# Kernel tuning notes

Hardware: AMD Instinct MI355X
Metric: run time of the kernel (lower is better)

The kernel has to match this reference:

```python
import jax, jax.numpy as jnp
import numpy as np

N = 10000
E = 80000


def gat_layer(x, src, dst, W, a_src, a_dst, b):
    # x: [N, Fin], W: [Fin, Fout]
    xw = x @ W                              # [N, Fout]
    al_src = xw @ a_src                     # [N]
    al_dst = xw @ a_dst                     # [N]
    e = jax.nn.leaky_relu(al_src[src] + al_dst[dst], 0.2)  # [E+N]
    m = jax.lax.stop_gradient(jax.ops.segment_max(e, dst, num_segments=N))
    ex = jnp.exp(e - m[dst])
    denom = jax.ops.segment_sum(ex, dst, num_segments=N)
    alpha = ex / (denom[dst] + 1e-16)       # PyG softmax eps
    out = jax.ops.segment_sum(alpha[:, None] * xw[src], dst, num_segments=N)
    return out + b


def setup_inputs() -> dict:
    key = jax.random.key(0)
    ks = jax.random.split(key, 12)
    x = jax.random.normal(ks[0], (N, 256), dtype=jnp.float32)
    edge_index = jax.random.randint(ks[1], (2, E), 0, N, dtype=jnp.int64)
    def glorot(k, fi, fo):
        return jax.random.normal(k, (fi, fo), jnp.float32) * jnp.sqrt(2.0 / (fi + fo))
    W1 = glorot(ks[2], 256, 2048)
    W2 = glorot(ks[3], 2048, 2048)
    W3 = glorot(ks[4], 2048, 1024)
    a1s = jax.random.normal(ks[5], (2048,), jnp.float32) * 0.05
    a1d = jax.random.normal(ks[6], (2048,), jnp.float32) * 0.05
    a2s = jax.random.normal(ks[7], (2048,), jnp.float32) * 0.05
    a2d = jax.random.normal(ks[8], (2048,), jnp.float32) * 0.05
    a3s = jax.random.normal(ks[9], (1024,), jnp.float32) * 0.05
    a3d = jax.random.normal(ks[10], (1024,), jnp.float32) * 0.05
    b1 = jnp.zeros((2048,), jnp.float32)
    b2 = jnp.zeros((2048,), jnp.float32)
    b3 = jnp.zeros((1024,), jnp.float32)
    return {"x": x, "edge_index": edge_index, "W1": W1, "W2": W2, "W3": W3,
            "a1s": a1s, "a1d": a1d, "a2s": a2s, "a2d": a2d, "a3s": a3s, "a3d": a3d,
            "b1": b1, "b2": b2, "b3": b3}


def reference(x, edge_index, W1, W2, W3, a1s, a1d, a2s, a2d, a3s, a3d, b1, b2, b3):
    # add self loops (PyG GATConv default add_self_loops=True)
    loop = jnp.arange(N, dtype=edge_index.dtype)
    src = jnp.concatenate([edge_index[0], loop])
    dst = jnp.concatenate([edge_index[1], loop])
    h = jax.nn.relu(gat_layer(x, src, dst, W1, a1s, a1d, b1))
    h = jax.nn.relu(gat_layer(h, src, dst, W2, a2s, a2d, b2))
    h = jax.nn.relu(gat_layer(h, src, dst, W3, a3s, a3d, b3))
    # F.normalize(dim=1), eps=1e-12
    norm = jnp.linalg.norm(h, axis=1, keepdims=True)
    return h / jnp.maximum(norm, 1e-12)
```

## Files before the change

kernel.cpp:

```cpp
#include <hip/hip_runtime.h>
#include <hip/hip_bf16.h>
#include <math.h>


typedef __attribute__((ext_vector_type(8))) short short8;
typedef __attribute__((ext_vector_type(4))) float f32x4;

#define GLOAD_LDS16(g, l)                                            \
  __builtin_amdgcn_global_load_lds(                                  \
      (const __attribute__((address_space(1))) void*)(g),            \
      (__attribute__((address_space(3))) void*)(l), 16, 0, 0)

__device__ __forceinline__ float bf16_to_f32(ushort u) {
  return __uint_as_float(((unsigned int)u) << 16);
}

__device__ __forceinline__ float block_reduce_sum_bcast(float v) {
#pragma unroll
  for (int off = 32; off > 0; off >>= 1) v += __shfl_down(v, off, 64);
  __shared__ float tmp[4];
  __shared__ float res;
  int lane = threadIdx.x & 63, w = threadIdx.x >> 6;
  if (lane == 0) tmp[w] = v;
  __syncthreads();
  if (threadIdx.x == 0) res = tmp[0] + tmp[1] + tmp[2] + tmp[3];
  __syncthreads();
  float out = res;
  __syncthreads();
  return out;
}

__device__ __forceinline__ float block_reduce_max_bcast(float v) {
#pragma unroll
  for (int off = 32; off > 0; off >>= 1) v = fmaxf(v, __shfl_down(v, off, 64));
  __shared__ float tmpm[4];
  __shared__ float resm;
  int lane = threadIdx.x & 63, w = threadIdx.x >> 6;
  if (lane == 0) tmpm[w] = v;
  __syncthreads();
  if (threadIdx.x == 0) resm = fmaxf(fmaxf(tmpm[0], tmpm[1]), fmaxf(tmpm[2], tmpm[3]));
  __syncthreads();
  float out = resm;
  __syncthreads();
  return out;
}

__global__ void detect_kernel(const int* __restrict__ ei32, int* __restrict__ flag) {
  __shared__ int cnt;
  if (threadIdx.x == 0) cnt = 0;
  __syncthreads();
  int zeros = 0;
  for (int i = threadIdx.x; i < 1024; i += 256) {
    if (ei32[2 * i + 1] == 0) zeros++;
  }
  atomicAdd(&cnt, zeros);
  __syncthreads();
  if (threadIdx.x == 0) *flag = (cnt > 900) ? 1 : 0;
}

__global__ void convert_kernel(const void* __restrict__ ei, const int* __restrict__ flag,
                               int E, int* __restrict__ src, int* __restrict__ dst) {
  int i = blockIdx.x * blockDim.x + threadIdx.x;
  if (i >= E) return;
  if (*flag) {
    const long long* p = (const long long*)ei;
    src[i] = (int)p[i];
    dst[i] = (int)p[E + i];
  } else {
    const int* p = (const int*)ei;
    src[i] = p[i];
    dst[i] = p[E + i];
  }
}

__global__ __launch_bounds__(256) void convert_f32_bf16(const float* __restrict__ in,
                                                        __hip_bfloat16* __restrict__ out,
                                                        int n) {
  int i = blockIdx.x * blockDim.x + threadIdx.x;
  if (i < n) out[i] = __float2bfloat16(in[i]);
}

__global__ __launch_bounds__(256) void transpose_w(const float* __restrict__ W,
                                                   __hip_bfloat16* __restrict__ Wt,
                                                   int K, int Nout) {
  __shared__ float t[32][33];
  int tx = threadIdx.x & 31, ty = threadIdx.x >> 5;
  int n0 = blockIdx.x * 32, k0 = blockIdx.y * 32;
#pragma unroll
  for (int i = 0; i < 4; ++i) {
    int k = k0 + ty + i * 8;
    t[ty + i * 8][tx] = W[(size_t)k * Nout + n0 + tx];
  }
  __syncthreads();
#pragma unroll
  for (int i = 0; i < 4; ++i) {
    int n = n0 + ty + i * 8;
    Wt[(size_t)n * K + k0 + tx] = __float2bfloat16(t[tx][ty + i * 8]);
  }
}

__global__ __launch_bounds__(256) void matvec_wa(const float* __restrict__ W,
                                                 const float* __restrict__ a_s,
                                                 const float* __restrict__ a_d,
                                                 float* __restrict__ wa_s,
                                                 float* __restrict__ wa_d, int F) {
  int k = blockIdx.x;
  const float* row = W + (size_t)k * F;
  float s1 = 0.f, s2 = 0.f;
  for (int f = threadIdx.x; f < F; f += 256) {
    float w = row[f];
    s1 += w * a_s[f];
    s2 += w * a_d[f];
  }
  float r1 = block_reduce_sum_bcast(s1);
  float r2 = block_reduce_sum_bcast(s2);
  if (threadIdx.x == 0) {
    wa_s[k] = r1;
    wa_d[k] = r2;
  }
}

template <int FPT>
__global__ __launch_bounds__(256) void compute_al(const ushort* __restrict__ H,
                                                  const float* __restrict__ wa_s,
                                                  const float* __restrict__ wa_d,
                                                  float* __restrict__ als,
                                                  float* __restrict__ ald, int F) {
  int n = blockIdx.x;
  const ushort* row = H + (size_t)n * F;
  float s1 = 0.f, s2 = 0.f;
  if (FPT == 8) {
    int base = threadIdx.x * 8;
    short8 v = *(const short8*)(row + base);
#pragma unroll
    for (int j = 0; j < 8; ++j) {
      float f = bf16_to_f32((ushort)v[j]);
      s1 += f * wa_s[base + j];
      s2 += f * wa_d[base + j];
    }
  } else {
    float f = bf16_to_f32(row[threadIdx.x]);
    s1 = f * wa_s[threadIdx.x];
    s2 = f * wa_d[threadIdx.x];
  }
  float r1 = block_reduce_sum_bcast(s1);
  float r2 = block_reduce_sum_bcast(s2);
  if (threadIdx.x == 0) {
    als[n] = r1;
    ald[n] = r2;
  }
}

__global__ void count_kernel(const int* __restrict__ dst, int* __restrict__ counts, int E) {
  int i = blockIdx.x * blockDim.x + threadIdx.x;
  if (i < E) atomicAdd(&counts[dst[i]], 1);
}

__global__ __launch_bounds__(1024) void scan_kernel(const int* __restrict__ counts,
                                                    int* __restrict__ rowptr,
                                                    int* __restrict__ cursor, int Nn) {
  __shared__ int part[1024];
  int tid = threadIdx.x;
  int chunk = (Nn + 1023) / 1024;
  int base = tid * chunk;
  int s = 0;
  for (int i = 0; i < chunk; ++i) {
    int idx = base + i;
    if (idx < Nn) s += counts[idx];
  }
  part[tid] = s;
  __syncthreads();
  for (int off = 1; off < 1024; off <<= 1) {
    int v = 0;
    if (tid >= off) v = part[tid - off];
    __syncthreads();
    if (tid >= off) part[tid] += v;
    __syncthreads();
  }
  int run = (tid == 0) ? 0 : part[tid - 1];
  for (int i = 0; i < chunk; ++i) {
    int idx = base + i;
    if (idx < Nn) {
      rowptr[idx] = run;
      cursor[idx] = run;
      run += counts[idx];
    }
  }
  if (tid == 1023) rowptr[Nn] = part[1023];
}

__global__ void fill_kernel(const int* __restrict__ src, const int* __restrict__ dst,
                            int* __restrict__ cursor, int* __restrict__ eidx, int E) {
  int i = blockIdx.x * blockDim.x + threadIdx.x;
  if (i < E) {
    int pos = atomicAdd(&cursor[dst[i]], 1);
    eidx[pos] = src[i];
  }
}

template <int FPT>
__global__ __launch_bounds__(256) void aggregate(const ushort* __restrict__ H,
                                                 const float* __restrict__ als,
                                                 const float* __restrict__ ald,
                                                 const int* __restrict__ rowptr,
                                                 const int* __restrict__ eidx,
                                                 ushort* __restrict__ out, int F) {
  int n = blockIdx.x;
  int tid = threadIdx.x;
  int beg = rowptr[n], end = rowptr[n + 1];
  int deg = end - beg;
  float aldn = ald[n];

  float lm = -INFINITY;
  for (int j = tid; j < deg; j += 256) {
    int s = eidx[beg + j];
    float e = als[s] + aldn;
    e = (e > 0.f) ? e : 0.2f * e;
    lm = fmaxf(lm, e);
  }
  if (tid == 0) {
    float e = als[n] + aldn;
    e = (e > 0.f) ? e : 0.2f * e;
    lm = fmaxf(lm, e);
  }
  float m = block_reduce_max_bcast(lm);

  float ls = 0.f;
  for (int j = tid; j < deg; j += 256) {
    int s = eidx[beg + j];
    float e = als[s] + aldn;
    e = (e > 0.f) ? e : 0.2f * e;
    ls += expf(e - m);
  }
  if (tid == 0) {
    float e = als[n] + aldn;
    e = (e > 0.f) ? e : 0.2f * e;
    ls += expf(e - m);
  }
  float denom = block_reduce_sum_bcast(ls) + 1e-16f;
  float inv_denom = 1.f / denom;

  float acc[FPT];
#pragma unroll
  for (int i = 0; i < FPT; ++i) acc[i] = 0.f;

  __shared__ float alpha_sh[256];
  __shared__ int src_sh[256];
  int total = deg + 1;
  for (int c0 = 0; c0 < total; c0 += 256) {
    int j = c0 + tid;
    if (j < total) {
      int s = (j < deg) ? eidx[beg + j] : n;
      float e = als[s] + aldn;
      e = (e > 0.f) ? e : 0.2f * e;
      alpha_sh[tid] = expf(e - m) * inv_denom;
      src_sh[tid] = s;
    }
    __syncthreads();
    int cn = min(256, total - c0);
    for (int jj = 0; jj < cn; ++jj) {
      float al = alpha_sh[jj];
      const ushort* row = H + (size_t)src_sh[jj] * F;
      if (FPT == 1) {
        acc[0] += al * bf16_to_f32(row[tid]);
      } else {
#pragma unroll
        for (int i = 0; i < FPT / 2; ++i) {
          unsigned int u = *(const unsigned int*)(row + tid * 2 + i * 512);
          acc[2 * i]     += al * __uint_as_float((u & 0xffffu) << 16);
          acc[2 * i + 1] += al * __uint_as_float(u & 0xffff0000u);
        }
      }
    }
    __syncthreads();
  }

#pragma unroll
  for (int i = 0; i < FPT; ++i) {
    int col = (FPT == 1) ? tid : (tid * 2 + (i >> 1) * 512 + (i & 1));
    __hip_bfloat16 hv = __float2bfloat16(acc[i]);
    out[(size_t)n * F + col] = *(ushort*)&hv;
  }
}

template <bool BF16OUT>
__global__ __launch_bounds__(512, 2) void gemm_bn128(const ushort* __restrict__ A,
                                                     const ushort* __restrict__ Bt,
                                                     const float* __restrict__ bias,
                                                     void* __restrict__ C,
                                                     int M, int K, int Nout) {
  constexpr int BUF = 16384 + 8192;
  extern __shared__ ushort lds[];
  const int tid = threadIdx.x;
  const int l = tid & 63, w = tid >> 6;
  const int wm = w >> 2, wn = w & 3;
  const int l15 = l & 15, lhi = l >> 4;

  int nwg = gridDim.x * gridDim.y;
  int lin = blockIdx.y * gridDim.x + blockIdx.x;
  if ((nwg & 7) == 0) lin = (lin & 7) * (nwg >> 3) + (lin >> 3);
  const int bx = lin % gridDim.x, by = lin / gridDim.x;
  const int row0 = by * 256, col0 = bx * 128;

  const int c8sw = (l & 3) ^ (((l >> 5) & 1) << 1);
  const int lrow = l >> 2;
  const int chsw = lhi ^ (((l15 >> 3) & 1) << 1);
  const int rd_off = l15 * 32 + chsw * 8;

  const int sA0 = wm * 8 + wn * 2;
  const int sB0 = w;
  const ushort* ga[2][2];
  const ushort* gb[2];
#pragma unroll
  for (int sc = 0; sc < 2; ++sc) {
#pragma unroll
    for (int j = 0; j < 2; ++j) {
      int ar = min(row0 + (sA0 + j) * 16 + lrow, M - 1);
      ga[sc][j] = A + (size_t)ar * K + sc * 32 + c8sw * 8;
    }
    gb[sc] = Bt + (size_t)(col0 + sB0 * 16 + lrow) * K + sc * 32 + c8sw * 8;
  }

#define STAGE_PH(nb, kn, sc)                                                         \
  do {                                                                               \
    GLOAD_LDS16(ga[sc][0] + (kn), &lds[(nb)*BUF + ((sA0 + 0) * 2 + (sc)) * 512]);    \
    GLOAD_LDS16(ga[sc][1] + (kn), &lds[(nb)*BUF + ((sA0 + 1) * 2 + (sc)) * 512]);    \
    GLOAD_LDS16(gb[sc] + (kn), &lds[(nb)*BUF + 16384 + (sB0 * 2 + (sc)) * 512]);     \
  } while (0)

  f32x4 acc[8][2] = {};

#define PHASE(cbase, kk, STAGE_STMT)                                                 \
  do {                                                                               \
    short8 af[8], bf[2];                                                             \
    _Pragma("unroll") for (int m = 0; m < 8; ++m)                                    \
        af[m] = *(const short8*)(cbase + ((wm * 8 + m) * 2 + (kk)) * 512 + rd_off);  \
    _Pragma("unroll") for (int n = 0; n < 2; ++n)                                    \
        bf[n] = *(const short8*)(cbase + 16384 + ((wn * 2 + n) * 2 + (kk)) * 512 + rd_off); \
    STAGE_STMT;                                                                      \
    asm volatile("s_waitcnt vmcnt(6)" ::: "memory");                                 \
    __builtin_amdgcn_s_barrier();                                                    \
    __builtin_amdgcn_s_setprio(1);                                                   \
    _Pragma("unroll") for (int m = 0; m < 8; ++m)                                    \
        _Pragma("unroll") for (int n = 0; n < 2; ++n)                                \
            acc[m][n] = __builtin_amdgcn_mfma_f32_16x16x32_bf16(                     \
                af[m], bf[n], acc[m][n], 0, 0, 0);                                   \
    __builtin_amdgcn_s_setprio(0);                                                   \
    __builtin_amdgcn_s_barrier();                                                    \
  } while (0)

  const int nt = K >> 6;
  STAGE_PH(0, 0, 0);
  STAGE_PH(0, 0, 1);
  STAGE_PH(1, 64, 0);
  STAGE_PH(1, 64, 1);
  asm volatile("s_waitcnt vmcnt(6)" ::: "memory");
  __builtin_amdgcn_s_barrier();

  int cur = 0;
  for (int t = 0; t < nt; ++t) {
    const ushort* cb = &lds[cur * BUF];
    int nb = cur + 2; if (nb >= 3) nb -= 3;
    const bool pf = (t + 2) < nt;
    const int kn = (t + 2) << 6;
    PHASE(cb, 0, if (pf) STAGE_PH(nb, kn, 0));
    PHASE(cb, 1, if (pf) STAGE_PH(nb, kn, 1));
    cur = cur + 1; if (cur == 3) cur = 0;
  }

#pragma unroll
  for (int mi = 0; mi < 8; ++mi) {
#pragma unroll
    for (int v = 0; v < 4; ++v) {
      int r = row0 + wm * 128 + mi * 16 + lhi * 4 + v;
      if (r < M) {
#pragma unroll
        for (int n = 0; n < 2; ++n) {
          int col = col0 + wn * 32 + n * 16 + l15;
          float val = fmaxf(acc[mi][n][v] + bias[col], 0.f);
          size_t idx = (size_t)r * Nout + col;
          if (BF16OUT)
            ((__hip_bfloat16*)C)[idx] = __float2bfloat16(val);
          else
            ((float*)C)[idx] = val;
        }
      }
    }
  }
#undef PHASE
#undef STAGE_PH
}

__global__ __launch_bounds__(256) void normalize_kernel(const float* __restrict__ h,
                                                        float* __restrict__ out,
                                                        int F) {
  int n = blockIdx.x;
  const float* row = h + (size_t)n * F;
  float ss = 0.f;
  for (int f = threadIdx.x; f < F; f += 256) {
    float v = row[f];
    ss += v * v;
  }
  float tot = block_reduce_sum_bcast(ss);
  float inv = 1.f / fmaxf(sqrtf(tot), 1e-12f);
  for (int f = threadIdx.x; f < F; f += 256) {
    out[(size_t)n * F + f] = row[f] * inv;
  }
}

extern "C" void kernel_launch(void* const* d_in, const int* in_sizes, int n_in,
                              void* d_out, int out_size, void* d_ws, size_t ws_size,
                              hipStream_t stream) {
  const float* x   = (const float*)d_in[0];
  const void*  ei  = d_in[1];
  const float* W1  = (const float*)d_in[2];
  const float* W2  = (const float*)d_in[3];
  const float* W3  = (const float*)d_in[4];
  const float* a1s = (const float*)d_in[5];
  const float* a1d = (const float*)d_in[6];
  const float* a2s = (const float*)d_in[7];
  const float* a2d = (const float*)d_in[8];
  const float* a3s = (const float*)d_in[9];
  const float* a3d = (const float*)d_in[10];
  const float* b1  = (const float*)d_in[11];
  const float* b2  = (const float*)d_in[12];
  const float* b3  = (const float*)d_in[13];

  const int N = in_sizes[0] / 256;
  const int E = in_sizes[1] / 2;

  char* ws = (char*)d_ws;
  size_t off = 0;
  auto alloc = [&](size_t bytes) -> void* {
    void* p = ws + off;
    off += (bytes + 255) & ~(size_t)255;
    return p;
  };
  ushort* h    = (ushort*)alloc((size_t)N * 2048 * 2);
  ushort* hagg = (ushort*)alloc((size_t)N * 2048 * 2);
  float* hf32  = (float*)alloc((size_t)N * 1024 * 4);
  ushort* xb   = (ushort*)alloc((size_t)N * 256 * 2);
  __hip_bfloat16* Wt1 = (__hip_bfloat16*)alloc((size_t)2048 * 256 * 2);
  __hip_bfloat16* Wt2 = (__hip_bfloat16*)alloc((size_t)2048 * 2048 * 2);
  __hip_bfloat16* Wt3 = (__hip_bfloat16*)alloc((size_t)1024 * 2048 * 2);
  float* wa1s = (float*)alloc(256 * 4);
  float* wa1d = (float*)alloc(256 * 4);
  float* wa2s = (float*)alloc(2048 * 4);
  float* wa2d = (float*)alloc(2048 * 4);
  float* wa3s = (float*)alloc(2048 * 4);
  float* wa3d = (float*)alloc(2048 * 4);
  float* als   = (float*)alloc((size_t)N * 4);
  float* ald   = (float*)alloc((size_t)N * 4);
  int* counts  = (int*)alloc((size_t)N * 4);
  int* rowptr  = (int*)alloc((size_t)(N + 1) * 4);
  int* cursor  = (int*)alloc((size_t)N * 4);
  int* eidx    = (int*)alloc((size_t)E * 4);
  int* src32   = (int*)alloc((size_t)E * 4);
  int* dst32   = (int*)alloc((size_t)E * 4);
  int* flag    = (int*)alloc(256);

  static bool attr_done = false;
  if (!attr_done) {
    hipFuncSetAttribute((const void*)gemm_bn128<true>,
                        hipFuncAttributeMaxDynamicSharedMemorySize, 147456);
    hipFuncSetAttribute((const void*)gemm_bn128<false>,
                        hipFuncAttributeMaxDynamicSharedMemorySize, 147456);
    attr_done = true;
  }

  detect_kernel<<<1, 256, 0, stream>>>((const int*)ei, flag);
  convert_kernel<<<(E + 255) / 256, 256, 0, stream>>>(ei, flag, E, src32, dst32);
  hipMemsetAsync(counts, 0, (size_t)N * 4, stream);
  count_kernel<<<(E + 255) / 256, 256, 0, stream>>>(dst32, counts, E);
  scan_kernel<<<1, 1024, 0, stream>>>(counts, rowptr, cursor, N);
  fill_kernel<<<(E + 255) / 256, 256, 0, stream>>>(src32, dst32, cursor, eidx, E);

  convert_f32_bf16<<<(N * 256 + 255) / 256, 256, 0, stream>>>(x, (__hip_bfloat16*)xb, N * 256);
  transpose_w<<<dim3(2048 / 32, 256 / 32), 256, 0, stream>>>(W1, Wt1, 256, 2048);
  transpose_w<<<dim3(2048 / 32, 2048 / 32), 256, 0, stream>>>(W2, Wt2, 2048, 2048);
  transpose_w<<<dim3(1024 / 32, 2048 / 32), 256, 0, stream>>>(W3, Wt3, 2048, 1024);
  matvec_wa<<<256, 256, 0, stream>>>(W1, a1s, a1d, wa1s, wa1d, 2048);
  matvec_wa<<<2048, 256, 0, stream>>>(W2, a2s, a2d, wa2s, wa2d, 2048);
  matvec_wa<<<2048, 256, 0, stream>>>(W3, a3s, a3d, wa3s, wa3d, 1024);

  dim3 blk(256);
  dim3 gblk(512);
  int mb = (N + 255) / 256;

  compute_al<1><<<N, blk, 0, stream>>>(xb, wa1s, wa1d, als, ald, 256);
  aggregate<1><<<N, blk, 0, stream>>>(xb, als, ald, rowptr, eidx, hagg, 256);
  gemm_bn128<true><<<dim3(2048 / 128, mb), gblk, 147456, stream>>>(hagg, (const ushort*)Wt1, b1, h, N, 256, 2048);

  compute_al<8><<<N, blk, 0, stream>>>(h, wa2s, wa2d, als, ald, 2048);
  aggregate<8><<<N, blk, 0, stream>>>(h, als, ald, rowptr, eidx, hagg, 2048);
  gemm_bn128<true><<<dim3(2048 / 128, mb), gblk, 147456, stream>>>(hagg, (const ushort*)Wt2, b2, h, N, 2048, 2048);

  compute_al<8><<<N, blk, 0, stream>>>(h, wa3s, wa3d, als, ald, 2048);
  aggregate<8><<<N, blk, 0, stream>>>(h, als, ald, rowptr, eidx, hagg, 2048);
  gemm_bn128<false><<<dim3(1024 / 128, mb), gblk, 147456, stream>>>(hagg, (const ushort*)Wt3, b3, hf32, N, 2048, 1024);

  normalize_kernel<<<N, blk, 0, stream>>>(hf32, (float*)d_out, 1024);
}
```

Baseline: 473.9 us.

## Restructure GEMM pipeline to five-stage K=32 buffers with deeper prefetch

Replaces the three-buffer, K=64-per-stage GEMM pipeline (two phases per stage) with a five-buffer ring of K=32 stages, prefetching four stages ahead. The barrier and vmcnt wait now come before the LDS fragment reads, and the tail phases use decreasing wait counts. The goal is more loads in flight and less time stalled on global-to-LDS latency. The cost is a per-block LDS size (122880 bytes) that still permits only one block per CU (launch bounds changed to 1), and one barrier pair per 32-wide K step.

```diff
diff --git a/kernel.cpp b/kernel.cpp
--- a/kernel.cpp
+++ b/kernel.cpp
@@ -10,6 +10,8 @@
   __builtin_amdgcn_global_load_lds(                                  \
       (const __attribute__((address_space(1))) void*)(g),            \
       (__attribute__((address_space(3))) void*)(l), 16, 0, 0)
+
+#define CFENCE asm volatile("" ::: "memory")
 
 __device__ __forceinline__ float bf16_to_f32(ushort u) {
   return __uint_as_float(((unsigned int)u) << 16);
@@ -284,12 +286,12 @@
 }
 
 template <bool BF16OUT>
-__global__ __launch_bounds__(512, 2) void gemm_bn128(const ushort* __restrict__ A,
-                                                     const ushort* __restrict__ Bt,
-                                                     const float* __restrict__ bias,
-                                                     void* __restrict__ C,
-                                                     int M, int K, int Nout) {
-  constexpr int BUF = 16384 + 8192;
+__global__ __launch_bounds__(512, 1) void gemm_p5(const ushort* __restrict__ A,
+                                                  const ushort* __restrict__ Bt,
+                                                  const float* __restrict__ bias,
+                                                  void* __restrict__ C,
+                                                  int M, int K, int Nout) {
+  constexpr int BUF = 12288;
   extern __shared__ ushort lds[];
   const int tid = threadIdx.x;
   const int l = tid & 63, w = tid >> 6;
@@ -307,66 +309,71 @@
   const int chsw = lhi ^ (((l15 >> 3) & 1) << 1);
   const int rd_off = l15 * 32 + chsw * 8;
 
-  const int sA0 = wm * 8 + wn * 2;
+  const int sA0 = w * 2;
   const int sB0 = w;
-  const ushort* ga[2][2];
-  const ushort* gb[2];
-#pragma unroll
-  for (int sc = 0; sc < 2; ++sc) {
-#pragma unroll
-    for (int j = 0; j < 2; ++j) {
-      int ar = min(row0 + (sA0 + j) * 16 + lrow, M - 1);
-      ga[sc][j] = A + (size_t)ar * K + sc * 32 + c8sw * 8;
-    }
-    gb[sc] = Bt + (size_t)(col0 + sB0 * 16 + lrow) * K + sc * 32 + c8sw * 8;
-  }
-
-#define STAGE_PH(nb, kn, sc)                                                         \
+  const ushort* ga[2];
+  const ushort* gb;
+#pragma unroll
+  for (int j = 0; j < 2; ++j) {
+    int ar = min(row0 + (sA0 + j) * 16 + lrow, M - 1);
+    ga[j] = A + (size_t)ar * K + c8sw * 8;
+  }
+  gb = Bt + (size_t)(col0 + sB0 * 16 + lrow) * K + c8sw * 8;
+
+#define STAGE(nb, kn)                                               \
+  do {                                                              \
+    GLOAD_LDS16(ga[0] + (kn), &lds[(nb)*BUF + (sA0 + 0) * 512]);    \
+    GLOAD_LDS16(ga[1] + (kn), &lds[(nb)*BUF + (sA0 + 1) * 512]);    \
+    GLOAD_LDS16(gb + (kn), &lds[(nb)*BUF + 8192 + sB0 * 512]);      \
+  } while (0)
+
+  f32x4 acc[8][2] = {};
+
+#define PHASE(cur, WAITLIT, STAGE_STMT)                                              \
   do {                                                                               \
-    GLOAD_LDS16(ga[sc][0] + (kn), &lds[(nb)*BUF + ((sA0 + 0) * 2 + (sc)) * 512]);    \
-    GLOAD_LDS16(ga[sc][1] + (kn), &lds[(nb)*BUF + ((sA0 + 1) * 2 + (sc)) * 512]);    \
-    GLOAD_LDS16(gb[sc] + (kn), &lds[(nb)*BUF + 16384 + (sB0 * 2 + (sc)) * 512]);     \
-  } while (0)
-
-  f32x4 acc[8][2] = {};
-
-#define PHASE(cbase, kk, STAGE_STMT)                                                 \
-  do {                                                                               \
+    STAGE_STMT;                                                                      \
+    asm volatile("s_waitcnt vmcnt(" WAITLIT ")" ::: "memory");                       \
+    __builtin_amdgcn_s_barrier();                                                    \
+    CFENCE;                                                                          \
     short8 af[8], bf[2];                                                             \
+    const ushort* Ab = &lds[(cur)*BUF];                                              \
+    const ushort* Bb = &lds[(cur)*BUF + 8192];                                       \
     _Pragma("unroll") for (int m = 0; m < 8; ++m)                                    \
-        af[m] = *(const short8*)(cbase + ((wm * 8 + m) * 2 + (kk)) * 512 + rd_off);  \
+        af[m] = *(const short8*)(Ab + (wm * 8 + m) * 512 + rd_off);                  \
     _Pragma("unroll") for (int n = 0; n < 2; ++n)                                    \
-        bf[n] = *(const short8*)(cbase + 16384 + ((wn * 2 + n) * 2 + (kk)) * 512 + rd_off); \
-    STAGE_STMT;                                                                      \
-    asm volatile("s_waitcnt vmcnt(6)" ::: "memory");                                 \
-    __builtin_amdgcn_s_barrier();                                                    \
+        bf[n] = *(const short8*)(Bb + (wn * 2 + n) * 512 + rd_off);                  \
     __builtin_amdgcn_s_setprio(1);                                                   \
     _Pragma("unroll") for (int m = 0; m < 8; ++m)                                    \
         _Pragma("unroll") for (int n = 0; n < 2; ++n)                                \
             acc[m][n] = __builtin_amdgcn_mfma_f32_16x16x32_bf16(                     \
                 af[m], bf[n], acc[m][n], 0, 0, 0);                                   \
     __builtin_amdgcn_s_setprio(0);                                                   \
+    CFENCE;                                                                          \
     __builtin_amdgcn_s_barrier();                                                    \
+    CFENCE;                                                                          \
   } while (0)
 
-  const int nt = K >> 6;
-  STAGE_PH(0, 0, 0);
-  STAGE_PH(0, 0, 1);
-  STAGE_PH(1, 64, 0);
-  STAGE_PH(1, 64, 1);
-  asm volatile("s_waitcnt vmcnt(6)" ::: "memory");
-  __builtin_amdgcn_s_barrier();
-
-  int cur = 0;
-  for (int t = 0; t < nt; ++t) {
-    const ushort* cb = &lds[cur * BUF];
-    int nb = cur + 2; if (nb >= 3) nb -= 3;
-    const bool pf = (t + 2) < nt;
-    const int kn = (t + 2) << 6;
-    PHASE(cb, 0, if (pf) STAGE_PH(nb, kn, 0));
-    PHASE(cb, 1, if (pf) STAGE_PH(nb, kn, 1));
-    cur = cur + 1; if (cur == 3) cur = 0;
-  }
+  const int nt = K >> 5;
+  STAGE(0, 0);
+  STAGE(1, 32);
+  STAGE(2, 64);
+  STAGE(3, 96);
+
+  int cur = 0, nb = 4;
+  int t = 0;
+  for (; t < nt - 4; ++t) {
+    const int kn = (t + 4) << 5;
+    PHASE(cur, "12", STAGE(nb, kn));
+    cur = (cur == 4) ? 0 : cur + 1;
+    nb = (nb == 4) ? 0 : nb + 1;
+  }
+  PHASE(cur, "9", );
+  cur = (cur == 4) ? 0 : cur + 1;
+  PHASE(cur, "6", );
+  cur = (cur == 4) ? 0 : cur + 1;
+  PHASE(cur, "3", );
+  cur = (cur == 4) ? 0 : cur + 1;
+  PHASE(cur, "0", );
 
 #pragma unroll
   for (int mi = 0; mi < 8; ++mi) {
@@ -388,7 +395,7 @@
     }
   }
 #undef PHASE
-#undef STAGE_PH
+#undef STAGE
 }
 
 __global__ __launch_bounds__(256) void normalize_kernel(const float* __restrict__ h,
@@ -461,10 +468,10 @@
 
   static bool attr_done = false;
   if (!attr_done) {
-    hipFuncSetAttribute((const void*)gemm_bn128<true>,
-                        hipFuncAttributeMaxDynamicSharedMemorySize, 147456);
-    hipFuncSetAttribute((const void*)gemm_bn128<false>,
-                        hipFuncAttributeMaxDynamicSharedMemorySize, 147456);
+    hipFuncSetAttribute((const void*)gemm_p5<true>,
+                        hipFuncAttributeMaxDynamicSharedMemorySize, 122880);
+    hipFuncSetAttribute((const void*)gemm_p5<false>,
+                        hipFuncAttributeMaxDynamicSharedMemorySize, 122880);
     attr_done = true;
   }
 
@@ -489,15 +496,15 @@
 
   compute_al<1><<<N, blk, 0, stream>>>(xb, wa1s, wa1d, als, ald, 256);
   aggregate<1><<<N, blk, 0, stream>>>(xb, als, ald, rowptr, eidx, hagg, 256);
-  gemm_bn128<true><<<dim3(2048 / 128, mb), gblk, 147456, stream>>>(hagg, (const ushort*)Wt1, b1, h, N, 256, 2048);
+  gemm_p5<true><<<dim3(2048 / 128, mb), gblk, 122880, stream>>>(hagg, (const ushort*)Wt1, b1, h, N, 256, 2048);
 
   compute_al<8><<<N, blk, 0, stream>>>(h, wa2s, wa2d, als, ald, 2048);
   aggregate<8><<<N, blk, 0, stream>>>(h, als, ald, rowptr, eidx, hagg, 2048);
-  gemm_bn128<true><<<dim3(2048 / 128, mb), gblk, 147456, stream>>>(hagg, (const ushort*)Wt2, b2, h, N, 2048, 2048);
+  gemm_p5<true><<<dim3(2048 / 128, mb), gblk, 122880, stream>>>(hagg, (const ushort*)Wt2, b2, h, N, 2048, 2048);
 
   compute_al<8><<<N, blk, 0, stream>>>(h, wa3s, wa3d, als, ald, 2048);
   aggregate<8><<<N, blk, 0, stream>>>(h, als, ald, rowptr, eidx, hagg, 2048);
-  gemm_bn128<false><<<dim3(1024 / 128, mb), gblk, 147456, stream>>>(hagg, (const ushort*)Wt3, b3, hf32, N, 2048, 1024);
+  gemm_p5<false><<<dim3(1024 / 128, mb), gblk, 122880, stream>>>(hagg, (const ushort*)Wt3, b3, hf32, N, 2048, 1024);
 
   normalize_kernel<<<N, blk, 0, stream>>>(hf32, (float*)d_out, 1024);
 }
```

New measurement: 483.8 us. 1.02x slower.
